# Performance work log

Hardware: AMD Instinct MI355X
Metric: run time of the kernel (lower is better)

## Reference

```python
import jax, jax.numpy as jnp
import numpy as np

OT_REG = 0.1
OT_ITERS = 10
LN_EPS = 1e-5


def layernorm(x, g, b):
    m = jnp.mean(x, axis=-1, keepdims=True)
    v = jnp.mean((x - m) ** 2, axis=-1, keepdims=True)
    return (x - m) * jax.lax.rsqrt(v + LN_EPS) * g + b


def sinkhorn(C, epsilon, iters):
    # standard Sinkhorn: kernel exp(C/eps), alternate row/col normalization
    Q = jnp.exp(C / epsilon)  # [Na,B,La,Lb]
    def body(_, Q):
        Q = Q / jnp.sum(Q, axis=-1, keepdims=True)
        Q = Q / jnp.sum(Q, axis=-2, keepdims=True)
        return Q
    return jax.lax.fori_loop(0, iters, body, Q)


def setup_inputs() -> dict:
    key = jax.random.key(0)
    ks = jax.random.split(key, 16)
    Na, La, B, Lb, Din, H = 32, 32, 64, 32, 768, 768
    s = 0.02
    return {
        "entity_cls": jax.random.normal(ks[0], (Na, Din), jnp.float32),
        "entity_tokens": jax.random.normal(ks[1], (Na, La, Din), jnp.float32),
        "mention_cls": jax.random.normal(ks[2], (B, Din), jnp.float32),
        "mention_tokens": jax.random.normal(ks[3], (B, Lb, Din), jnp.float32),
        "Wq": jax.random.normal(ks[4], (Din, H), jnp.float32) * s,
        "bq": jnp.zeros((H,), jnp.float32),
        "Wk": jax.random.normal(ks[5], (Din, H), jnp.float32) * s,
        "bk": jnp.zeros((H,), jnp.float32),
        "Wv": jax.random.normal(ks[6], (Din, H), jnp.float32) * s,
        "bv": jnp.zeros((H,), jnp.float32),
        "ln1_g": jnp.ones((H,), jnp.float32),
        "ln1_b": jnp.zeros((H,), jnp.float32),
        "Wcls": jax.random.normal(ks[7], (Din, H), jnp.float32) * s,
        "bcls": jnp.zeros((H,), jnp.float32),
        "Wsp": jax.random.normal(ks[8], (H, 1), jnp.float32) * s,
        "bsp": jnp.zeros((1,), jnp.float32),
        "ln2_g": jnp.ones((H,), jnp.float32),
        "ln2_b": jnp.zeros((H,), jnp.float32),
    }


def reference(entity_cls, entity_tokens, mention_cls, mention_tokens,
              Wq, bq, Wk, bk, Wv, bv, ln1_g, ln1_b,
              Wcls, bcls, Wsp, bsp, ln2_g, ln2_b):
    # projections
    q = entity_tokens @ Wq + bq      # [Na,La,H]
    k = mention_tokens @ Wk + bk     # [B,Lb,H]
    v = mention_tokens @ Wv + bv     # [B,Lb,H]

    # cross-batch cosine similarity: [Na,B,La,Lb]
    qn = q / jnp.maximum(jnp.linalg.norm(q, axis=-1, keepdims=True), 1e-8)
    kn = k / jnp.maximum(jnp.linalg.norm(k, axis=-1, keepdims=True), 1e-8)
    C = jnp.einsum('aid,bjd->abij', qn, kn)

    # Sinkhorn on detached cost (torch uses C.detach())
    T = sinkhorn(jax.lax.stop_gradient(C), OT_REG, OT_ITERS)
    # F.normalize(dim=-1): L2 normalize last dim
    T = T / jnp.maximum(jnp.linalg.norm(T, axis=-1, keepdims=True), 1e-12)

    # attention + residual + layernorm: [Na,B,La,H]
    attended = jnp.einsum('abij,bjd->abid', T, v) + q[:, None, :, :]
    attended = layernorm(attended, ln1_g, ln1_b)

    # softpool over token dim (-2)
    w = jax.nn.softmax(attended @ Wsp + bsp, axis=-2)   # [Na,B,La,1]
    pooled = jnp.sum(attended * w, axis=-2)             # [Na,B,H]
    context = layernorm(pooled, ln2_g, ln2_b)

    # matching scores
    ecls = entity_cls @ Wcls + bcls                     # [Na,H]
    g2l = jnp.sum(ecls[:, None, :] * context, axis=-1)  # [Na,B]
    g2l = g2l.T                                         # [B,Na]
    g2g = mention_cls @ entity_cls.T                    # [B,Na]
    return (g2l + g2g) * 0.5
```

## Files before the change

kernel.cpp:

```cpp
#include <hip/hip_runtime.h>
#include <math.h>


typedef __attribute__((ext_vector_type(8))) short bfrag8;
typedef __attribute__((ext_vector_type(4))) float f32x4;

__device__ __forceinline__ unsigned short f2bf(float x) {
  union { float f; unsigned u; } v; v.f = x;
  unsigned r = v.u + 0x7fffu + ((v.u >> 16) & 1u);
  return (unsigned short)(r >> 16);
}
__device__ __forceinline__ float bf2f(unsigned short x) {
  union { float f; unsigned u; } v; v.u = ((unsigned)x) << 16; return v.f;
}

template <int CTRL>
__device__ __forceinline__ float dpp_add(float x) {
  union { float f; int i; } a, b;
  a.f = x;
  b.i = __builtin_amdgcn_update_dpp(0, a.i, CTRL, 0xf, 0xf, true);
  return x + b.f;
}
__device__ __forceinline__ float sum16(float x) {
  x = dpp_add<0xB1>(x);
  x = dpp_add<0x4E>(x);
  x = dpp_add<0x124>(x);
  x = dpp_add<0x128>(x);
  return x;
}

__global__ __launch_bounds__(256) void prep_kernel(
    const float* __restrict__ a0, const float* __restrict__ a1, const float* __restrict__ a2,
    unsigned short* __restrict__ o0, unsigned short* __restrict__ o1, unsigned short* __restrict__ o2,
    float* __restrict__ nrm,
    const float* __restrict__ W0, const float* __restrict__ W1,
    const float* __restrict__ W2, const float* __restrict__ W3,
    unsigned short* __restrict__ T0, unsigned short* __restrict__ T1,
    unsigned short* __restrict__ T2, unsigned short* __restrict__ T3) {
  __shared__ float t[32][33];
  int bx = blockIdx.x;
  if (bx < 2331) {
    if (bx < 2328) {
      const float* in; unsigned short* out; int i, n4;
      if (bx < 768)       { in = a0; out = o0; i = bx * 256 + threadIdx.x;          n4 = 196608; }
      else if (bx < 2304) { in = a1; out = o1; i = (bx - 768) * 256 + threadIdx.x;  n4 = 393216; }
      else                { in = a2; out = o2; i = (bx - 2304) * 256 + threadIdx.x; n4 = 6144; }
      if (i >= n4) return;
      float4 f = ((const float4*)in)[i];
      ushort4 o;
      o.x = f2bf(f.x); o.y = f2bf(f.y); o.z = f2bf(f.z); o.w = f2bf(f.w);
      ((ushort4*)out)[i] = o;
    } else {
      int i = (bx - 2328) * 256 + threadIdx.x;
      if (i < 768) ((float4*)nrm)[i] = make_float4(0.f, 0.f, 0.f, 0.f);
    }
    return;
  }
  int idx = bx - 2331;
  int z = idx / 576, r2 = idx % 576;
  int tby = r2 / 24, tbx = r2 % 24;
  const float* W = (z == 0) ? W0 : (z == 1) ? W1 : (z == 2) ? W2 : W3;
  unsigned short* O = (z == 0) ? T0 : (z == 1) ? T1 : (z == 2) ? T2 : T3;
  const int gx = tbx * 32, gy = tby * 32;
  const int tx = threadIdx.x & 31, ty = threadIdx.x >> 5;
#pragma unroll
  for (int u = 0; u < 4; ++u) {
    int row = ty + u * 8;
    t[row][tx] = W[(size_t)(gy + row) * 768 + gx + tx];
  }
  __syncthreads();
#pragma unroll
  for (int u = 0; u < 4; ++u) {
    int row = ty + u * 8;
    O[(size_t)(gx + row) * 768 + gy + tx] = f2bf(t[tx][row]);
  }
}

__global__ __launch_bounds__(512, 2) void proj_gemm_kernel(
    const unsigned short* __restrict__ Ae, const unsigned short* __restrict__ Am,
    const unsigned short* __restrict__ Acls,
    const unsigned short* __restrict__ WqT, const unsigned short* __restrict__ WkT,
    const unsigned short* __restrict__ WvT, const unsigned short* __restrict__ WclsT,
    const float* __restrict__ bq, const float* __restrict__ bk,
    const float* __restrict__ bv, const float* __restrict__ bcls,
    unsigned short* __restrict__ qb, unsigned short* __restrict__ qT,
    unsigned short* __restrict__ kb, unsigned short* __restrict__ vT,
    float* __restrict__ ecls, float* __restrict__ iq_sq, float* __restrict__ ik_sq) {
  const int z = blockIdx.z;
  const int M = (z == 0) ? 1024 : (z == 3) ? 32 : 2048;
  const int bm = blockIdx.y * 128;
  if (bm >= M) return;
  const unsigned short* A = (z == 3) ? Acls : (z == 0) ? Ae : Am;
  const unsigned short* B = (z == 0) ? WqT : (z == 1) ? WkT : (z == 2) ? WvT : WclsT;
  const float* bias = (z == 0) ? bq : (z == 1) ? bk : (z == 2) ? bv : bcls;

  __shared__ unsigned short As[128 * 64];
  __shared__ unsigned short Bs[64 * 64];
  const int t = threadIdx.x;
  const int bn = blockIdx.x * 64;
  const int l = t & 63, w = t >> 6;
  const int wm = w & 3, wn = w >> 2;
  const int cg = l & 15, rq = l >> 4;

  f32x4 acc[2][2];
#pragma unroll
  for (int mi = 0; mi < 2; ++mi)
#pragma unroll
    for (int nj = 0; nj < 2; ++nj) { f32x4 zz = {0.f, 0.f, 0.f, 0.f}; acc[mi][nj] = zz; }

  for (int k0 = 0; k0 < 768; k0 += 64) {
    __syncthreads();
#pragma unroll
    for (int u = 0; u < 2; ++u) {
      int c = t + u * 512;
      int row = c >> 3, kc = c & 7;
      int gm = bm + row; gm = gm < M ? gm : M - 1;
      int4 av = *(const int4*)(A + (size_t)gm * 768 + k0 + kc * 8);
      *(int4*)(As + row * 64 + ((kc ^ (row & 7)) * 8)) = av;
    }
    {
      int row = t >> 3, kc = t & 7;
      int4 bv4 = *(const int4*)(B + (size_t)(bn + row) * 768 + k0 + kc * 8);
      *(int4*)(Bs + row * 64 + ((kc ^ (row & 7)) * 8)) = bv4;
    }
    __syncthreads();
#pragma unroll
    for (int kk = 0; kk < 2; ++kk) {
      bfrag8 af[2], bf[2];
      const int kc = kk * 4 + rq;
#pragma unroll
      for (int mi = 0; mi < 2; ++mi) {
        int arow = wm * 32 + mi * 16 + cg;
        af[mi] = *(const bfrag8*)(As + arow * 64 + ((kc ^ (arow & 7)) * 8));
      }
#pragma unroll
      for (int nj = 0; nj < 2; ++nj) {
        int brow = wn * 32 + nj * 16 + cg;
        bf[nj] = *(const bfrag8*)(Bs + brow * 64 + ((kc ^ (brow & 7)) * 8));
      }
#pragma unroll
      for (int mi = 0; mi < 2; ++mi)
#pragma unroll
        for (int nj = 0; nj < 2; ++nj)
          acc[mi][nj] = __builtin_amdgcn_mfma_f32_16x16x32_bf16(af[mi], bf[nj], acc[mi][nj], 0, 0, 0);
    }
  }

  float p[2][4] = {};
#pragma unroll
  for (int mi = 0; mi < 2; ++mi) {
#pragma unroll
    for (int nj = 0; nj < 2; ++nj) {
      int gn = bn + wn * 32 + nj * 16 + cg;
      float bs = bias[gn];
#pragma unroll
      for (int r = 0; r < 4; ++r) {
        int gm = bm + wm * 32 + mi * 16 + rq * 4 + r;
        if (gm >= M) continue;
        float val = acc[mi][nj][r] + bs;
        if (z < 2) p[mi][r] += val * val;
        unsigned short bfv = f2bf(val);
        if (z == 0) {
          qb[(size_t)gm * 768 + gn] = bfv;
          int at = gm >> 5, j = gm & 31;
          qT[((size_t)at * 768 + gn) * 32 + j] = bfv;
        } else if (z == 1) kb[(size_t)gm * 768 + gn] = bfv;
        else if (z == 2) {
          int bb = gm >> 5, j = gm & 31;
          vT[((size_t)bb * 768 + gn) * 32 + j] = bfv;
        } else ecls[(size_t)gm * 768 + gn] = val;
      }
    }
  }
  if (z < 2) {
    float* nrm = (z == 0) ? iq_sq : ik_sq;
#pragma unroll
    for (int mi = 0; mi < 2; ++mi)
#pragma unroll
      for (int r = 0; r < 4; ++r) {
        float s = sum16(p[mi][r]);
        if (cg == 0) {
          int gm = bm + wm * 32 + mi * 16 + rq * 4 + r;
          atomicAdd(&nrm[gm], s);
        }
      }
  }
}

__global__ __launch_bounds__(512, 2) void cos_attn_kernel(
    const unsigned short* __restrict__ qb, const unsigned short* __restrict__ kb,
    const float* __restrict__ iq_sq, const float* __restrict__ ik_sq,
    const unsigned short* __restrict__ qT,
    const unsigned short* __restrict__ vT,
    const float* __restrict__ ln1_g, const float* __restrict__ ln1_b,
    const float* __restrict__ Wsp, const float* __restrict__ bsp,
    const float* __restrict__ ln2_g, const float* __restrict__ ln2_b,
    const float* __restrict__ ecls,
    const float* __restrict__ entity_cls, const float* __restrict__ mention_cls,
    float* __restrict__ out) {
  __shared__ unsigned short vLds[2 * 768 * 32];
  __shared__ __align__(16) unsigned short scratch[12288];
  __shared__ float gabLds[4 * 768];
  __shared__ float gwLds[768];
  __shared__ float ldsIq[128], ldsIk[64];
  __shared__ float red[80];
  __shared__ __align__(16) unsigned short uLds[8 * 32];
  __shared__ __align__(16) unsigned short tvLds[8 * 32];

  unsigned short* As = scratch;
  unsigned short* Bs = scratch + 8192;
  unsigned short* Tlds = scratch;

  const int t = threadIdx.x;
  const int l = t & 63, w = t >> 6;
  const int bm = blockIdx.y * 128, bn = blockIdx.x * 64;
  const int wm = w & 3, wn = w >> 2;
  const int cg = l & 15, rq = l >> 4;

  {
    float sgw = 0.f, sbw = 0.f, sga[4] = {}, sba[4] = {};
    for (int h = t; h < 768; h += 512) {
      float g1 = ln1_g[h], b1 = ln1_b[h], wsp = Wsp[h];
      float g2 = ln2_g[h], b2 = ln2_b[h];
      float gw = g1 * wsp;
      gwLds[h] = gw;
      sgw += gw; sbw += b1 * wsp;
#pragma unroll
      for (int aa = 0; aa < 4; ++aa) {
        float ec = ecls[(size_t)((blockIdx.y << 2) + aa) * 768 + h];
        float gab = g2 * ec;
        gabLds[aa * 768 + h] = gab;
        sga[aa] += gab; sba[aa] += b2 * ec;
      }
    }
    sgw = sum16(sgw); sbw = sum16(sbw);
#pragma unroll
    for (int aa = 0; aa < 4; ++aa) { sga[aa] = sum16(sga[aa]); sba[aa] = sum16(sba[aa]); }
#pragma unroll
    for (int m = 16; m < 64; m <<= 1) {
      sgw += __shfl_xor(sgw, m); sbw += __shfl_xor(sbw, m);
#pragma unroll
      for (int aa = 0; aa < 4; ++aa) { sga[aa] += __shfl_xor(sga[aa], m); sba[aa] += __shfl_xor(sba[aa], m); }
    }
    if (l == 0) {
      red[w * 10 + 0] = sgw; red[w * 10 + 1] = sbw;
#pragma unroll
      for (int aa = 0; aa < 4; ++aa) { red[w * 10 + 2 + aa] = sga[aa]; red[w * 10 + 6 + aa] = sba[aa]; }
    }
  }
  if (t < 128) ldsIq[t] = iq_sq[bm + t];
  else if (t < 192) ldsIk[t - 128] = ik_sq[bn + t - 128];

  const int4* vsrc = (const int4*)(vT + (size_t)(blockIdx.x * 2) * 768 * 32);
  int4* vdst = (int4*)vLds;

  f32x4 acc[2][2];
#pragma unroll
  for (int mi = 0; mi < 2; ++mi)
#pragma unroll
    for (int nj = 0; nj < 2; ++nj) { f32x4 zz = {0.f, 0.f, 0.f, 0.f}; acc[mi][nj] = zz; }

  for (int k0 = 0, s = 0; k0 < 768; k0 += 64, ++s) {
    __syncthreads();
#pragma unroll
    for (int u = 0; u < 2; ++u) {
      int c = t + u * 512;
      int row = c >> 3, kc = c & 7;
      int4 av = *(const int4*)(qb + (size_t)(bm + row) * 768 + k0 + kc * 8);
      *(int4*)(As + row * 64 + ((kc ^ (row & 7)) * 8)) = av;
    }
    {
      int row = t >> 3, kc = t & 7;
      int4 bv4 = *(const int4*)(kb + (size_t)(bn + row) * 768 + k0 + kc * 8);
      *(int4*)(Bs + row * 64 + ((kc ^ (row & 7)) * 8)) = bv4;
    }
    vdst[t + s * 512] = vsrc[t + s * 512];
    __syncthreads();
#pragma unroll
    for (int kk = 0; kk < 2; ++kk) {
      bfrag8 af[2], bf[2];
      const int kc = kk * 4 + rq;
#pragma unroll
      for (int mi = 0; mi < 2; ++mi) {
        int arow = wm * 32 + mi * 16 + cg;
        af[mi] = *(const bfrag8*)(As + arow * 64 + ((kc ^ (arow & 7)) * 8));
      }
#pragma unroll
      for (int nj = 0; nj < 2; ++nj) {
        int brow = wn * 32 + nj * 16 + cg;
        bf[nj] = *(const bfrag8*)(Bs + brow * 64 + ((kc ^ (brow & 7)) * 8));
      }
#pragma unroll
      for (int mi = 0; mi < 2; ++mi)
#pragma unroll
        for (int nj = 0; nj < 2; ++nj)
          acc[mi][nj] = __builtin_amdgcn_mfma_f32_16x16x32_bf16(af[mi], bf[nj], acc[mi][nj], 0, 0, 0);
    }
  }

  float irow[2][4], icol[2];
#pragma unroll
  for (int mi = 0; mi < 2; ++mi)
#pragma unroll
    for (int r = 0; r < 4; ++r) {
      float sv = ldsIq[wm * 32 + mi * 16 + rq * 4 + r];
      irow[mi][r] = 1.0f / fmaxf(sqrtf(sv), 1e-8f);
    }
#pragma unroll
  for (int nj = 0; nj < 2; ++nj) {
    float sv = ldsIk[wn * 32 + nj * 16 + cg];
    icol[nj] = 1.0f / fmaxf(sqrtf(sv), 1e-8f);
  }
#pragma unroll
  for (int mi = 0; mi < 2; ++mi)
#pragma unroll
    for (int nj = 0; nj < 2; ++nj)
#pragma unroll
      for (int r = 0; r < 4; ++r)
        acc[mi][nj][r] = __expf(acc[mi][nj][r] * irow[mi][r] * icol[nj] * 10.0f);

  for (int it = 0; it < 10; ++it) {
#pragma unroll
    for (int mi = 0; mi < 2; ++mi)
#pragma unroll
      for (int r = 0; r < 4; ++r) {
        float rs = sum16(acc[mi][0][r] + acc[mi][1][r]);
        float rinv = __builtin_amdgcn_rcpf(rs);
        acc[mi][0][r] *= rinv; acc[mi][1][r] *= rinv;
      }
#pragma unroll
    for (int nj = 0; nj < 2; ++nj) {
      float cs = acc[0][nj][0] + acc[0][nj][1] + acc[0][nj][2] + acc[0][nj][3]
               + acc[1][nj][0] + acc[1][nj][1] + acc[1][nj][2] + acc[1][nj][3];
      cs += __shfl_xor(cs, 16); cs += __shfl_xor(cs, 32);
      float cinv = __builtin_amdgcn_rcpf(cs);
#pragma unroll
      for (int mi = 0; mi < 2; ++mi)
#pragma unroll
        for (int r = 0; r < 4; ++r) acc[mi][nj][r] *= cinv;
    }
  }

#pragma unroll
  for (int mi = 0; mi < 2; ++mi)
#pragma unroll
    for (int r = 0; r < 4; ++r) {
      float ss = sum16(acc[mi][0][r] * acc[mi][0][r] + acc[mi][1][r] * acc[mi][1][r]);
      float tinv = 1.0f / fmaxf(sqrtf(ss), 1e-12f);
      acc[mi][0][r] *= tinv; acc[mi][1][r] *= tinv;
    }

  __syncthreads();
  {
    unsigned short* base = Tlds + ((wn * 4 + wm) << 10);
#pragma unroll
    for (int mi = 0; mi < 2; ++mi)
#pragma unroll
      for (int nj = 0; nj < 2; ++nj)
#pragma unroll
        for (int r = 0; r < 4; ++r)
          base[(mi * 16 + rq * 4 + r) * 32 + nj * 16 + cg] = f2bf(acc[mi][nj][r]);
  }
  __syncthreads();

  const int bl = w & 1, ah = w >> 1;
  const int b_g = (blockIdx.x << 1) + bl;
  const int a_g = (blockIdx.y << 2) + ah;
  const unsigned short* vbase = vLds + bl * 24576;
  const int pairIdx = bl * 4 + ah;

  float sgw_f = 0.f, sbw_f = 0.f, sga_f = 0.f, sba_f = 0.f;
#pragma unroll
  for (int wv = 0; wv < 8; ++wv) {
    sgw_f += red[wv * 10 + 0]; sbw_f += red[wv * 10 + 1];
    sga_f += red[wv * 10 + 2 + ah]; sba_f += red[wv * 10 + 6 + ah];
  }
  sbw_f += bsp[0];

  const unsigned short* qTa = qT + (size_t)a_g * 24576;
  const unsigned short* Tp = Tlds + (pairIdx << 10);
  bfrag8 af[2], afI[2];
#pragma unroll
  for (int mi = 0; mi < 2; ++mi) {
    af[mi] = *(const bfrag8*)(Tp + (mi * 16 + cg) * 32 + rq * 8);
    int row = mi * 16 + cg;
    bfrag8 fI;
#pragma unroll
    for (int u = 0; u < 8; ++u) fI[u] = (row == rq * 8 + u) ? (short)0x3F80 : (short)0;
    afI[mi] = fI;
  }

  float s1[2][4] = {}, s2[2][4] = {}, a1[2][4] = {};
#pragma unroll 4
  for (int nj = 0; nj < 48; ++nj) {
    int h = nj * 16 + cg;
    bfrag8 vf = *(const bfrag8*)(vbase + h * 32 + rq * 8);
    bfrag8 qf = *(const bfrag8*)(qTa + (size_t)h * 32 + rq * 8);
    float gw = gwLds[h];
#pragma unroll
    for (int mi = 0; mi < 2; ++mi) {
      f32x4 zz = {0.f, 0.f, 0.f, 0.f};
      f32x4 p = __builtin_amdgcn_mfma_f32_16x16x32_bf16(af[mi], vf, zz, 0, 0, 0);
      f32x4 x4 = __builtin_amdgcn_mfma_f32_16x16x32_bf16(afI[mi], qf, p, 0, 0, 0);
#pragma unroll
      for (int r = 0; r < 4; ++r) {
        float x = x4[r];
        s1[mi][r] += x; s2[mi][r] += x * x; a1[mi][r] += x * gw;
      }
    }
  }
#pragma unroll
  for (int mi = 0; mi < 2; ++mi)
#pragma unroll
    for (int r = 0; r < 4; ++r) {
      s1[mi][r] = sum16(s1[mi][r]);
      s2[mi][r] = sum16(s2[mi][r]);
      a1[mi][r] = sum16(a1[mi][r]);
    }

  float uu[2][4], c0;
  {
    float mean[2][4], rstd[2][4], logit[2][4];
#pragma unroll
    for (int mi = 0; mi < 2; ++mi)
#pragma unroll
      for (int r = 0; r < 4; ++r) {
        float m1 = s1[mi][r] * (1.0f / 768.0f);
        float var = s2[mi][r] * (1.0f / 768.0f) - m1 * m1;
        float rs = rsqrtf(var + 1e-5f);
        mean[mi][r] = m1; rstd[mi][r] = rs;
        logit[mi][r] = rs * (a1[mi][r] - m1 * sgw_f) + sbw_f;
      }
    float mx = logit[0][0];
#pragma unroll
    for (int mi = 0; mi < 2; ++mi)
#pragma unroll
      for (int r = 0; r < 4; ++r) mx = fmaxf(mx, logit[mi][r]);
    mx = fmaxf(mx, __shfl_xor(mx, 16)); mx = fmaxf(mx, __shfl_xor(mx, 32));
    float se = 0.f, ee[2][4];
#pragma unroll
    for (int mi = 0; mi < 2; ++mi)
#pragma unroll
      for (int r = 0; r < 4; ++r) { ee[mi][r] = __expf(logit[mi][r] - mx); se += ee[mi][r]; }
    se += __shfl_xor(se, 16); se += __shfl_xor(se, 32);
    const float sinv = __builtin_amdgcn_rcpf(se);
    float c0a = 0.f;
#pragma unroll
    for (int mi = 0; mi < 2; ++mi)
#pragma unroll
      for (int r = 0; r < 4; ++r) {
        uu[mi][r] = ee[mi][r] * sinv * rstd[mi][r];
        c0a += uu[mi][r] * mean[mi][r];
      }
    c0a += __shfl_xor(c0a, 16); c0a += __shfl_xor(c0a, 32);
    c0 = c0a;
  }

  if (cg == 0) {
#pragma unroll
    for (int mi = 0; mi < 2; ++mi)
#pragma unroll
      for (int r = 0; r < 4; ++r)
        uLds[pairIdx * 32 + mi * 16 + rq * 4 + r] = f2bf(uu[mi][r]);
  }
  __syncthreads();
  {
    const int j = l & 31, ihalf = l >> 5;
    float tvp = 0.f;
#pragma unroll
    for (int ii = 0; ii < 16; ++ii) {
      int i = ihalf * 16 + ii;
      tvp += bf2f(uLds[pairIdx * 32 + i]) * bf2f(Tp[i * 32 + j]);
    }
    tvp += __shfl_xor(tvp, 32);
    if (l < 32) tvLds[pairIdx * 32 + j] = f2bf(tvp);
  }
  __syncthreads();
  bfrag8 afT, afQ;
  {
    bfrag8 z8;
#pragma unroll
    for (int u = 0; u < 8; ++u) z8[u] = 0;
    afT = z8; afQ = z8;
    if (cg == 0) {
      afT = *(const bfrag8*)(tvLds + pairIdx * 32 + rq * 8);
      afQ = *(const bfrag8*)(uLds + pairIdx * 32 + rq * 8);
    }
  }

  float ps = 0.f, pq = 0.f, spc = 0.f;
#pragma unroll 4
  for (int nj = 0; nj < 48; ++nj) {
    int h = nj * 16 + cg;
    bfrag8 vf = *(const bfrag8*)(vbase + h * 32 + rq * 8);
    bfrag8 qf = *(const bfrag8*)(qTa + (size_t)h * 32 + rq * 8);
    f32x4 z1 = {0.f, 0.f, 0.f, 0.f};
    f32x4 z2 = {0.f, 0.f, 0.f, 0.f};
    f32x4 pv = __builtin_amdgcn_mfma_f32_16x16x32_bf16(afT, vf, z1, 0, 0, 0);
    f32x4 pu = __builtin_amdgcn_mfma_f32_16x16x32_bf16(afQ, qf, z2, 0, 0, 0);
    float x = pv[0] + pu[0];
    float pooled = ln1_g[h] * (x - c0) + ln1_b[h];
    ps += pooled; pq += pooled * pooled;
    spc += pooled * gabLds[ah * 768 + h];
  }
  ps = sum16(ps); pq = sum16(pq); spc = sum16(spc);
  const float m2 = ps * (1.0f / 768.0f);
  const float var2 = pq * (1.0f / 768.0f) - m2 * m2;
  const float rs2 = rsqrtf(var2 + 1e-5f);
  const float* ea = entity_cls + (size_t)a_g * 768;
  const float* mb = mention_cls + (size_t)b_g * 768;
  float sg = 0.f;
#pragma unroll
  for (int u = 0; u < 12; ++u) sg += mb[l * 12 + u] * ea[l * 12 + u];
  sg = sum16(sg);
  sg += __shfl_xor(sg, 16); sg += __shfl_xor(sg, 32);
  float tot = rs2 * (spc - m2 * sga_f) + sba_f + sg;
  if (l == 0) out[b_g * 32 + a_g] = 0.5f * tot;
}

extern "C" void kernel_launch(void* const* d_in, const int* in_sizes, int n_in,
                              void* d_out, int out_size, void* d_ws, size_t ws_size,
                              hipStream_t stream) {
  const float* entity_cls     = (const float*)d_in[0];
  const float* entity_tokens  = (const float*)d_in[1];
  const float* mention_cls    = (const float*)d_in[2];
  const float* mention_tokens = (const float*)d_in[3];
  const float* Wq = (const float*)d_in[4];   const float* bq = (const float*)d_in[5];
  const float* Wk = (const float*)d_in[6];   const float* bk = (const float*)d_in[7];
  const float* Wv = (const float*)d_in[8];   const float* bv = (const float*)d_in[9];
  const float* ln1_g = (const float*)d_in[10]; const float* ln1_b = (const float*)d_in[11];
  const float* Wcls = (const float*)d_in[12];  const float* bcls = (const float*)d_in[13];
  const float* Wsp = (const float*)d_in[14];   const float* bsp = (const float*)d_in[15];
  const float* ln2_g = (const float*)d_in[16]; const float* ln2_b = (const float*)d_in[17];
  float* out = (float*)d_out;

  float* ws     = (float*)d_ws;
  float* ecls   = ws;
  float* iq_sq  = ecls + 24576;
  float* ik_sq  = iq_sq + 1024;
  unsigned short* qb = (unsigned short*)(ws + 55168);
  unsigned short* qT = qb + 786432;
  unsigned short* kb = qT + 786432;
  unsigned short* vT = kb + 1572864;
  char* R = (char*)(vT + 1572864);
  unsigned short* Ae    = (unsigned short*)R;
  unsigned short* Am    = Ae + 786432;
  unsigned short* Acls  = Am + 1572864;
  unsigned short* WqT   = Acls + 24576;
  unsigned short* WkT   = WqT + 589824;
  unsigned short* WvT   = WkT + 589824;
  unsigned short* WclsT = WvT + 589824;

  prep_kernel<<<dim3(4635), dim3(256), 0, stream>>>(
      entity_tokens, mention_tokens, entity_cls, Ae, Am, Acls, iq_sq,
      Wq, Wk, Wv, Wcls, WqT, WkT, WvT, WclsT);
  proj_gemm_kernel<<<dim3(12, 16, 4), dim3(512), 0, stream>>>(
      Ae, Am, Acls, WqT, WkT, WvT, WclsT, bq, bk, bv, bcls,
      qb, qT, kb, vT, ecls, iq_sq, ik_sq);
  cos_attn_kernel<<<dim3(32, 8), dim3(512), 0, stream>>>(
      qb, kb, iq_sq, ik_sq, qT, vT,
      ln1_g, ln1_b, Wsp, bsp, ln2_g, ln2_b,
      ecls, entity_cls, mention_cls, out);
}
```

Baseline: 163.0 us.

## Split cos_attn blocks to one mention per 256-thread block, shrink LDS

Each cos_attn block now handles one mention (b) and four entities with 4 waves instead of two mentions with 8 waves, doubling the grid to 64x8 and halving the V tile held in LDS. The gabLds table is removed; ln2_g*ecls is computed on the fly from global memory in the pooling loop. The aim is lower LDS use per block and more resident blocks for better occupancy and latency hiding. In exchange, the Q tile is loaded twice as often across blocks, and the final loop does extra global loads.

```diff
diff --git a/kernel.cpp b/kernel.cpp
--- a/kernel.cpp
+++ b/kernel.cpp
@@ -187,7 +187,7 @@
   }
 }
 
-__global__ __launch_bounds__(512, 2) void cos_attn_kernel(
+__global__ __launch_bounds__(256, 4) void cos_attn_kernel(
     const unsigned short* __restrict__ qb, const unsigned short* __restrict__ kb,
     const float* __restrict__ iq_sq, const float* __restrict__ ik_sq,
     const unsigned short* __restrict__ qT,
@@ -198,14 +198,13 @@
     const float* __restrict__ ecls,
     const float* __restrict__ entity_cls, const float* __restrict__ mention_cls,
     float* __restrict__ out) {
-  __shared__ unsigned short vLds[2 * 768 * 32];
-  __shared__ __align__(16) unsigned short scratch[12288];
-  __shared__ float gabLds[4 * 768];
+  __shared__ unsigned short vLds[768 * 32];
+  __shared__ __align__(16) unsigned short scratch[10240];
   __shared__ float gwLds[768];
-  __shared__ float ldsIq[128], ldsIk[64];
-  __shared__ float red[80];
-  __shared__ __align__(16) unsigned short uLds[8 * 32];
-  __shared__ __align__(16) unsigned short tvLds[8 * 32];
+  __shared__ float ldsIq[128], ldsIk[32];
+  __shared__ float red[40];
+  __shared__ __align__(16) unsigned short uLds[4 * 32];
+  __shared__ __align__(16) unsigned short tvLds[4 * 32];
 
   unsigned short* As = scratch;
   unsigned short* Bs = scratch + 8192;
@@ -213,13 +212,13 @@
 
   const int t = threadIdx.x;
   const int l = t & 63, w = t >> 6;
-  const int bm = blockIdx.y * 128, bn = blockIdx.x * 64;
-  const int wm = w & 3, wn = w >> 2;
+  const int bm = blockIdx.y * 128;
+  const int b_g = blockIdx.x;
   const int cg = l & 15, rq = l >> 4;
 
   {
     float sgw = 0.f, sbw = 0.f, sga[4] = {}, sba[4] = {};
-    for (int h = t; h < 768; h += 512) {
+    for (int h = t; h < 768; h += 256) {
       float g1 = ln1_g[h], b1 = ln1_b[h], wsp = Wsp[h];
       float g2 = ln2_g[h], b2 = ln2_b[h];
       float gw = g1 * wsp;
@@ -228,9 +227,7 @@
 #pragma unroll
       for (int aa = 0; aa < 4; ++aa) {
         float ec = ecls[(size_t)((blockIdx.y << 2) + aa) * 768 + h];
-        float gab = g2 * ec;
-        gabLds[aa * 768 + h] = gab;
-        sga[aa] += gab; sba[aa] += b2 * ec;
+        sga[aa] += g2 * ec; sba[aa] += b2 * ec;
       }
     }
     sgw = sum16(sgw); sbw = sum16(sbw);
@@ -249,9 +246,9 @@
     }
   }
   if (t < 128) ldsIq[t] = iq_sq[bm + t];
-  else if (t < 192) ldsIk[t - 128] = ik_sq[bn + t - 128];
-
-  const int4* vsrc = (const int4*)(vT + (size_t)(blockIdx.x * 2) * 768 * 32);
+  else if (t < 160) ldsIk[t - 128] = ik_sq[b_g * 32 + (t - 128)];
+
+  const int4* vsrc = (const int4*)(vT + (size_t)b_g * 768 * 32);
   int4* vdst = (int4*)vLds;
 
   f32x4 acc[2][2];
@@ -263,18 +260,18 @@
   for (int k0 = 0, s = 0; k0 < 768; k0 += 64, ++s) {
     __syncthreads();
 #pragma unroll
-    for (int u = 0; u < 2; ++u) {
-      int c = t + u * 512;
+    for (int u = 0; u < 4; ++u) {
+      int c = t + u * 256;
       int row = c >> 3, kc = c & 7;
       int4 av = *(const int4*)(qb + (size_t)(bm + row) * 768 + k0 + kc * 8);
       *(int4*)(As + row * 64 + ((kc ^ (row & 7)) * 8)) = av;
     }
     {
       int row = t >> 3, kc = t & 7;
-      int4 bv4 = *(const int4*)(kb + (size_t)(bn + row) * 768 + k0 + kc * 8);
+      int4 bv4 = *(const int4*)(kb + (size_t)(b_g * 32 + row) * 768 + k0 + kc * 8);
       *(int4*)(Bs + row * 64 + ((kc ^ (row & 7)) * 8)) = bv4;
     }
-    vdst[t + s * 512] = vsrc[t + s * 512];
+    vdst[t + s * 256] = vsrc[t + s * 256];
     __syncthreads();
 #pragma unroll
     for (int kk = 0; kk < 2; ++kk) {
@@ -282,12 +279,12 @@
       const int kc = kk * 4 + rq;
 #pragma unroll
       for (int mi = 0; mi < 2; ++mi) {
-        int arow = wm * 32 + mi * 16 + cg;
+        int arow = w * 32 + mi * 16 + cg;
         af[mi] = *(const bfrag8*)(As + arow * 64 + ((kc ^ (arow & 7)) * 8));
       }
 #pragma unroll
       for (int nj = 0; nj < 2; ++nj) {
-        int brow = wn * 32 + nj * 16 + cg;
+        int brow = nj * 16 + cg;
         bf[nj] = *(const bfrag8*)(Bs + brow * 64 + ((kc ^ (brow & 7)) * 8));
       }
 #pragma unroll
@@ -303,12 +300,12 @@
   for (int mi = 0; mi < 2; ++mi)
 #pragma unroll
     for (int r = 0; r < 4; ++r) {
-      float sv = ldsIq[wm * 32 + mi * 16 + rq * 4 + r];
+      float sv = ldsIq[w * 32 + mi * 16 + rq * 4 + r];
       irow[mi][r] = 1.0f / fmaxf(sqrtf(sv), 1e-8f);
     }
 #pragma unroll
   for (int nj = 0; nj < 2; ++nj) {
-    float sv = ldsIk[wn * 32 + nj * 16 + cg];
+    float sv = ldsIk[nj * 16 + cg];
     icol[nj] = 1.0f / fmaxf(sqrtf(sv), 1e-8f);
   }
 #pragma unroll
@@ -352,7 +349,7 @@
 
   __syncthreads();
   {
-    unsigned short* base = Tlds + ((wn * 4 + wm) << 10);
+    unsigned short* base = Tlds + (w << 10);
 #pragma unroll
     for (int mi = 0; mi < 2; ++mi)
 #pragma unroll
@@ -363,22 +360,18 @@
   }
   __syncthreads();
 
-  const int bl = w & 1, ah = w >> 1;
-  const int b_g = (blockIdx.x << 1) + bl;
-  const int a_g = (blockIdx.y << 2) + ah;
-  const unsigned short* vbase = vLds + bl * 24576;
-  const int pairIdx = bl * 4 + ah;
+  const int a_g = (blockIdx.y << 2) + w;
 
   float sgw_f = 0.f, sbw_f = 0.f, sga_f = 0.f, sba_f = 0.f;
 #pragma unroll
-  for (int wv = 0; wv < 8; ++wv) {
+  for (int wv = 0; wv < 4; ++wv) {
     sgw_f += red[wv * 10 + 0]; sbw_f += red[wv * 10 + 1];
-    sga_f += red[wv * 10 + 2 + ah]; sba_f += red[wv * 10 + 6 + ah];
+    sga_f += red[wv * 10 + 2 + w]; sba_f += red[wv * 10 + 6 + w];
   }
   sbw_f += bsp[0];
 
   const unsigned short* qTa = qT + (size_t)a_g * 24576;
-  const unsigned short* Tp = Tlds + (pairIdx << 10);
+  const unsigned short* Tp = Tlds + (w << 10);
   bfrag8 af[2], afI[2];
 #pragma unroll
   for (int mi = 0; mi < 2; ++mi) {
@@ -394,7 +387,7 @@
 #pragma unroll 4
   for (int nj = 0; nj < 48; ++nj) {
     int h = nj * 16 + cg;
-    bfrag8 vf = *(const bfrag8*)(vbase + h * 32 + rq * 8);
+    bfrag8 vf = *(const bfrag8*)(vLds + h * 32 + rq * 8);
     bfrag8 qf = *(const bfrag8*)(qTa + (size_t)h * 32 + rq * 8);
     float gw = gwLds[h];
 #pragma unroll
@@ -461,7 +454,7 @@
     for (int mi = 0; mi < 2; ++mi)
 #pragma unroll
       for (int r = 0; r < 4; ++r)
-        uLds[pairIdx * 32 + mi * 16 + rq * 4 + r] = f2bf(uu[mi][r]);
+        uLds[w * 32 + mi * 16 + rq * 4 + r] = f2bf(uu[mi][r]);
   }
   __syncthreads();
   {
@@ -470,10 +463,10 @@
 #pragma unroll
     for (int ii = 0; ii < 16; ++ii) {
       int i = ihalf * 16 + ii;
-      tvp += bf2f(uLds[pairIdx * 32 + i]) * bf2f(Tp[i * 32 + j]);
+      tvp += bf2f(uLds[w * 32 + i]) * bf2f(Tp[i * 32 + j]);
     }
     tvp += __shfl_xor(tvp, 32);
-    if (l < 32) tvLds[pairIdx * 32 + j] = f2bf(tvp);
+    if (l < 32) tvLds[w * 32 + j] = f2bf(tvp);
   }
   __syncthreads();
   bfrag8 afT, afQ;
@@ -483,16 +476,17 @@
     for (int u = 0; u < 8; ++u) z8[u] = 0;
     afT = z8; afQ = z8;
     if (cg == 0) {
-      afT = *(const bfrag8*)(tvLds + pairIdx * 32 + rq * 8);
-      afQ = *(const bfrag8*)(uLds + pairIdx * 32 + rq * 8);
-    }
-  }
-
+      afT = *(const bfrag8*)(tvLds + w * 32 + rq * 8);
+      afQ = *(const bfrag8*)(uLds + w * 32 + rq * 8);
+    }
+  }
+
+  const float* eca = ecls + (size_t)a_g * 768;
   float ps = 0.f, pq = 0.f, spc = 0.f;
 #pragma unroll 4
   for (int nj = 0; nj < 48; ++nj) {
     int h = nj * 16 + cg;
-    bfrag8 vf = *(const bfrag8*)(vbase + h * 32 + rq * 8);
+    bfrag8 vf = *(const bfrag8*)(vLds + h * 32 + rq * 8);
     bfrag8 qf = *(const bfrag8*)(qTa + (size_t)h * 32 + rq * 8);
     f32x4 z1 = {0.f, 0.f, 0.f, 0.f};
     f32x4 z2 = {0.f, 0.f, 0.f, 0.f};
@@ -501,7 +495,7 @@
     float x = pv[0] + pu[0];
     float pooled = ln1_g[h] * (x - c0) + ln1_b[h];
     ps += pooled; pq += pooled * pooled;
-    spc += pooled * gabLds[ah * 768 + h];
+    spc += pooled * (ln2_g[h] * eca[h]);
   }
   ps = sum16(ps); pq = sum16(pq); spc = sum16(spc);
   const float m2 = ps * (1.0f / 768.0f);
@@ -557,7 +551,7 @@
   proj_gemm_kernel<<<dim3(12, 16, 4), dim3(512), 0, stream>>>(
       Ae, Am, Acls, WqT, WkT, WvT, WclsT, bq, bk, bv, bcls,
       qb, qT, kb, vT, ecls, iq_sq, ik_sq);
-  cos_attn_kernel<<<dim3(32, 8), dim3(512), 0, stream>>>(
+  cos_attn_kernel<<<dim3(64, 8), dim3(256), 0, stream>>>(
       qb, kb, iq_sq, ik_sq, qT, vT,
       ln1_g, ln1_b, Wsp, bsp, ln2_g, ln2_b,
       ecls, entity_cls, mention_cls, out);
```

Result: no change. 162.7 us (-0.2%).
